# Kernel optimization log

Measured on AMD Instinct MI355X. Metric: run time of the kernel, lower is better.

The kernel has to match this reference:

```python
import jax, jax.numpy as jnp
import numpy as np

N = 200000          # number of nodes (objects)
H = 64              # hidden_size
ARITIES = [1, 2, 3] # arity per relation
NTUP = [250000, 250000, 250000]  # ground atoms per relation


def setup_inputs() -> dict:
    key = jax.random.key(0)
    ks = jax.random.split(key, 32)
    inp = {"node_states": jax.random.normal(ks[0], (N, H), jnp.float32)}
    i = 1
    for r, (a, t) in enumerate(zip(ARITIES, NTUP)):
        inp[f"rel{r}_idx"] = jax.random.randint(ks[i], (t * a,), 0, N, dtype=jnp.int32).astype(jnp.int64); i += 1
        d = a * H
        s = (2.0 / d) ** 0.5
        inp[f"w1_r{r}"] = jax.random.normal(ks[i], (d, d), jnp.float32) * s; i += 1
        inp[f"b1_r{r}"] = jnp.zeros((d,), jnp.float32)
        inp[f"w2_r{r}"] = jax.random.normal(ks[i], (d, d), jnp.float32) * s; i += 1
        inp[f"b2_r{r}"] = jnp.zeros((d,), jnp.float32)
    su = (1.0 / (2 * H)) ** 0.5
    inp["wu1"] = jax.random.normal(ks[i], (2 * H, 2 * H), jnp.float32) * su; i += 1
    inp["bu1"] = jnp.zeros((2 * H,), jnp.float32)
    inp["wu2"] = jax.random.normal(ks[i], (2 * H, H), jnp.float32) * su
    inp["bu2"] = jnp.zeros((H,), jnp.float32)
    return inp


def reference(node_states, rel0_idx, rel1_idx, rel2_idx,
              w1_r0, b1_r0, w2_r0, b2_r0,
              w1_r1, b1_r1, w2_r1, b2_r1,
              w1_r2, b1_r2, w2_r2, b2_r2,
              wu1, bu1, wu2, bu2):
    sum_msg = jnp.zeros_like(node_states)
    rels = [(ARITIES[0], rel0_idx, w1_r0, b1_r0, w2_r0, b2_r0),
            (ARITIES[1], rel1_idx, w1_r1, b1_r1, w2_r1, b2_r1),
            (ARITIES[2], rel2_idx, w1_r2, b1_r2, w2_r2, b2_r2)]
    for a, idx, w1, b1, w2, b2 in rels:
        # gather node states for each ground atom: [T, a*H]
        x = node_states[idx].reshape(-1, a * H)
        h = jax.nn.relu(x @ w1 + b1)
        msg = (h @ w2 + b2).reshape(-1, H)  # [T*a, H]
        # scatter-add messages back to their nodes
        sum_msg = sum_msg.at[idx].add(msg)
    z = jnp.concatenate([sum_msg, node_states], axis=1)  # [N, 2H]
    return jax.nn.relu(z @ wu1 + bu1) @ wu2 + bu2
```

## Files before the change

kernel.cpp:

```cpp
#include <hip/hip_runtime.h>

#define H 64

typedef __attribute__((ext_vector_type(8))) __bf16 bf16x8;
typedef __attribute__((ext_vector_type(4))) float f32x4;
typedef unsigned short u16;
typedef unsigned int u32;

union F8 { bf16x8 b; u16 u[8]; uint4 q; };

__device__ __forceinline__ u16 f2bf(float f) {
    union { __bf16 h; u16 u; } v; v.h = (__bf16)f; return v.u;
}
__device__ __forceinline__ float bf2f(u16 x) {
    return __uint_as_float((u32)x << 16);
}
__device__ __forceinline__ unsigned swz(int col, int k, int K) {
    return ((unsigned)(col * K + k) * 2u) ^ (((unsigned)col & 7u) << 4);
}

struct Seg { const float* src; unsigned dstBytes; int K; int N; };
struct Segs { Seg s[8]; };

__global__ __launch_bounds__(256) void conv_weights(Segs segs, char* out) {
    Seg sg = segs.s[blockIdx.y];
    int total = sg.K * sg.N;
    char* dst = out + sg.dstBytes;
    for (int e = blockIdx.x * 256 + threadIdx.x; e < total; e += gridDim.x * 256) {
        int k = e / sg.N, n = e % sg.N;
        *(u16*)(dst + swz(n, k, sg.K)) = f2bf(sg.src[e]);
    }
}

__global__ __launch_bounds__(256) void conv_nodes(const float4* __restrict__ src,
                                                  ushort4* __restrict__ dst, int n4) {
    for (int i = blockIdx.x * 256 + threadIdx.x; i < n4; i += gridDim.x * 256) {
        float4 f = src[i];
        ushort4 o;
        o.x = f2bf(f.x); o.y = f2bf(f.y); o.z = f2bf(f.z); o.w = f2bf(f.w);
        dst[i] = o;
    }
}

__global__ __launch_bounds__(512) void scan_blocks(u32* __restrict__ data,
                                                   u32* __restrict__ sums, int n) {
    __shared__ u32 s[512];
    int tid = threadIdx.x, i = blockIdx.x * 512 + tid;
    u32 v = (i < n) ? data[i] : 0u;
    s[tid] = v; __syncthreads();
    for (int d = 1; d < 512; d <<= 1) {
        u32 t = (tid >= d) ? s[tid - d] : 0u; __syncthreads();
        s[tid] += t; __syncthreads();
    }
    if (i < n) data[i] = s[tid] - v;
    if (tid == 511) sums[blockIdx.x] = s[511];
}

__global__ __launch_bounds__(512) void scan_sums(u32* __restrict__ sums, int nb) {
    __shared__ u32 s[512];
    int tid = threadIdx.x;
    u32 v = (tid < nb) ? sums[tid] : 0u;
    s[tid] = v; __syncthreads();
    for (int d = 1; d < 512; d <<= 1) {
        u32 t = (tid >= d) ? s[tid - d] : 0u; __syncthreads();
        s[tid] += t; __syncthreads();
    }
    if (tid < nb) sums[tid] = s[tid] - v;
}

__global__ __launch_bounds__(512) void scan_add(u32* __restrict__ data,
                                                const u32* __restrict__ sums, int n) {
    int i = blockIdx.x * 512 + threadIdx.x;
    if (i < n) data[i] += sums[blockIdx.x];
}

struct OFix {
    const int* idx0; const int* idx1; const int* idx2;
    int m0, m1, m2;
    const u32* base; const u32* pre; u32* ord;
};

__global__ __launch_bounds__(256) void ord_fix(OFix a) {
    const int Mtot = a.m0 + a.m1 + a.m2;
    for (int e = blockIdx.x * 256 + threadIdx.x; e < Mtot; e += gridDim.x * 256) {
        int lm = e, node;
        if (lm < a.m0) node = a.idx0[lm];
        else { lm -= a.m0; if (lm < a.m1) node = a.idx1[lm]; else node = a.idx2[lm - a.m1]; }
        a.ord[a.base[node] + a.pre[e]] = (u32)e;
    }
}

struct Scat {
    const int* idx0; const int* idx1; const int* idx2;
    int m0, m1, m2;
    const u32* base; const u32* pre;
    const u16* msgu; u16* msgs;
};

__global__ __launch_bounds__(256) void scatter_msg(Scat a) {
    const int Mtot = a.m0 + a.m1 + a.m2;
    const int CH = Mtot * 8;
    for (int c = blockIdx.x * 256 + threadIdx.x; c < CH; c += gridDim.x * 256) {
        const int e = c >> 3, q = c & 7;
        int lm = e, node;
        if (lm < a.m0) node = a.idx0[lm];
        else { lm -= a.m0; if (lm < a.m1) node = a.idx1[lm]; else node = a.idx2[lm - a.m1]; }
        const u32 slot = a.base[node] + a.pre[e];
        ((uint4*)(a.msgs + (size_t)slot * 64))[q] =
            ((const uint4*)(a.msgu + (size_t)e * 64))[q];
    }
}

template<int A>
__device__ __forceinline__ void msg_body(
    const u16* __restrict__ nsb, const int* __restrict__ idx,
    const u16* __restrict__ w1T, const float* __restrict__ b1,
    const u16* __restrict__ w2T, const float* __restrict__ b2,
    u16* __restrict__ msgR, int T, int bid, u16* Wl, u16* h1)
{
    constexpr int D    = A * 64;
    constexpr int KS   = D / 32;
    constexpr int NT   = D / 16;
    constexpr bool DUAL = (A == 1);
    constexpr bool CS   = (A > 1);
    constexpr int RF   = CS ? 2 : 1;
    constexpr int WH   = (A == 3) ? 3 : 1;
    constexpr int NTH  = NT / WH;
    constexpr int NTW  = CS ? NTH / 2 : NTH;
    constexpr int COLH = D / WH;
    constexpr int NPF  = (DUAL ? 2 * D * D : COLH * D) / 8 / 512;
    constexpr int NB   = WH * NTW;

    const int tid  = threadIdx.x;
    const int lane = tid & 63;
    const int w    = tid >> 6;
    const int g    = lane >> 4;
    const int lr   = lane & 15;
    const int rg   = CS ? (w >> 1) : w;
    const int cg   = CS ? (w & 1) : 0;

    const int tile = bid * 128;

    auto stage = [&](const u16* gsrc) {
#pragma unroll
        for (int i = 0; i < NPF; ++i) {
            const u16* gp = gsrc + ((i * 512 + tid) << 3);
            u16* lp = Wl + ((i * 512 + (w << 6)) << 3);
            __builtin_amdgcn_global_load_lds(
                (const __attribute__((address_space(1))) void*)gp,
                (__attribute__((address_space(3))) void*)lp, 16, 0, 0);
        }
    };

    bf16x8 a1[RF][KS];
#pragma unroll
    for (int rf = 0; rf < RF; ++rf) {
        const int trow = tile + rg * (16 * RF) + rf * 16 + lr;
        const int tl   = trow < T ? trow : T - 1;
        int nodes[A];
#pragma unroll
        for (int s = 0; s < A; ++s) nodes[s] = idx[(long)tl * A + s];
#pragma unroll
        for (int kk = 0; kk < KS; ++kk) {
            const u16* p = nsb + (long)nodes[kk >> 1] * H + ((kk & 1) * 32 + g * 8);
            F8 t; t.q = *(const uint4*)p;
            a1[rf][kk] = t.b;
        }
    }

    float bias1[NB], bias2[NB];
#pragma unroll
    for (int i = 0; i < NB; ++i) {
        const int jg = (i / NTW) * NTH + cg * NTW + (i % NTW);
        bias1[i] = b1[jg * 16 + lr];
        bias2[i] = b2[jg * 16 + lr];
    }

#pragma unroll
    for (int hh = 0; hh < WH; ++hh) {
        stage(DUAL ? w1T : (w1T + (size_t)hh * COLH * D));
        asm volatile("s_waitcnt vmcnt(0)" ::: "memory");
        __syncthreads();

#pragma unroll
        for (int jl = 0; jl < NTW; ++jl) {
            const int jc = cg * NTW + jl;
            const int jg = hh * NTH + jc;
            f32x4 acc0 = {0.f, 0.f, 0.f, 0.f};
            f32x4 acc1 = {0.f, 0.f, 0.f, 0.f};
#pragma unroll
            for (int kk = 0; kk < KS; ++kk) {
                F8 bf; bf.q = *(const uint4*)((const char*)Wl + swz(jc * 16 + lr, kk * 32 + g * 8, D));
                acc0 = __builtin_amdgcn_mfma_f32_16x16x32_bf16(a1[0][kk], bf.b, acc0, 0, 0, 0);
                if constexpr (CS)
                    acc1 = __builtin_amdgcn_mfma_f32_16x16x32_bf16(a1[1][kk], bf.b, acc1, 0, 0, 0);
            }
#pragma unroll
            for (int r = 0; r < 4; ++r) {
                const int row0 = rg * (16 * RF) + g * 4 + r;
                float v0 = acc0[r] + bias1[hh * NTW + jl]; v0 = v0 > 0.f ? v0 : 0.f;
                *(u16*)((char*)h1 + swz(row0, jg * 16 + lr, D)) = f2bf(v0);
                if constexpr (CS) {
                    float v1 = acc1[r] + bias1[hh * NTW + jl]; v1 = v1 > 0.f ? v1 : 0.f;
                    *(u16*)((char*)h1 + swz(row0 + 16, jg * 16 + lr, D)) = f2bf(v1);
                }
            }
        }
        if constexpr (!DUAL) __syncthreads();
    }

    bf16x8 a2[RF][KS];
#pragma unroll
    for (int rf = 0; rf < RF; ++rf) {
        const int row = rg * (16 * RF) + rf * 16 + lr;
#pragma unroll
        for (int kk = 0; kk < KS; ++kk) {
            F8 t; t.q = *(const uint4*)((const char*)h1 + swz(row, kk * 32 + g * 8, D));
            a2[rf][kk] = t.b;
        }
    }

#pragma unroll
    for (int hh = 0; hh < WH; ++hh) {
        if constexpr (!DUAL) {
            stage(w2T + (size_t)hh * COLH * D);
            asm volatile("s_waitcnt vmcnt(0)" ::: "memory");
            __syncthreads();
        }
        const char* W2base = DUAL ? (const char*)(Wl + D * D) : (const char*)Wl;

#pragma unroll
        for (int jl = 0; jl < NTW; ++jl) {
            const int jc = cg * NTW + jl;
            const int jg = hh * NTH + jc;
            f32x4 acc0 = {0.f, 0.f, 0.f, 0.f};
            f32x4 acc1 = {0.f, 0.f, 0.f, 0.f};
#pragma unroll
            for (int kk = 0; kk < KS; ++kk) {
                F8 bf; bf.q = *(const uint4*)(W2base + swz(jc * 16 + lr, kk * 32 + g * 8, D));
                acc0 = __builtin_amdgcn_mfma_f32_16x16x32_bf16(a2[0][kk], bf.b, acc0, 0, 0, 0);
                if constexpr (CS)
                    acc1 = __builtin_amdgcn_mfma_f32_16x16x32_bf16(a2[1][kk], bf.b, acc1, 0, 0, 0);
            }
            const int gc   = jg * 16 + lr;
            const int slot = gc >> 6;
            const int cs_  = gc & 63;
#pragma unroll
            for (int r = 0; r < 4; ++r) {
                const int a0 = rg * (16 * RF) + g * 4 + r;
                const int m0 = a0 * A + slot;
                unsigned b0 = (((unsigned)(m0 * 64 + cs_)) * 2u) ^ (((unsigned)m0 & 7u) << 4);
                *(u16*)((char*)h1 + b0) = f2bf(acc0[r] + bias2[hh * NTW + jl]);
                if constexpr (CS) {
                    const int m1 = (a0 + 16) * A + slot;
                    unsigned b1x = (((unsigned)(m1 * 64 + cs_)) * 2u) ^ (((unsigned)m1 & 7u) << 4);
                    *(u16*)((char*)h1 + b1x) = f2bf(acc1[r] + bias2[hh * NTW + jl]);
                }
            }
        }
        if constexpr (!DUAL) { if (hh + 1 < WH) __syncthreads(); }
    }

    if constexpr (CS) {
        __syncthreads();
        const int mbase = tile * A;
        constexpr int CH = 128 * A * 16;
#pragma unroll
        for (int i = 0; i < CH / 512; ++i) {
            const int c    = i * 512 + tid;
            const int row  = c >> 4;
            const int atom = row / A;
            if (tile + atom < T) {
                unsigned byte = (((unsigned)(row * 64 + (c & 15) * 4)) * 2u) ^ (((unsigned)row & 7u) << 4);
                uint2 v = *(const uint2*)((const char*)h1 + byte);
                *(uint2*)(msgR + (size_t)(mbase + row) * 64 + (c & 15) * 4) = v;
            }
        }
    } else {
        const bool full  = (tile + 128 <= T);
#pragma unroll
        for (int i = 0; i < 16 * A; i += 4) {
            int ml   = i + (lane >> 4);
            int mrow = w * 16 * A + ml;
            bool ok  = full || ((tile + w * 16 + ml / A) < T);
            if (ok) {
                unsigned byte = (((unsigned)(mrow * 64 + (lane & 15) * 4)) * 2u) ^ (((unsigned)mrow & 7u) << 4);
                uint2 v = *(const uint2*)((const char*)h1 + byte);
                *(uint2*)(msgR + (size_t)((tile * A) + mrow) * 64 + (lane & 15) * 4) = v;
            }
        }
    }
}

struct MegaA {
    const u16* nsb;
    const int* idx0; const int* idx1; const int* idx2;
    int m0, m1, m2, t0, t1, t2;
    u32* cnt; u32* pre;
    const u16 *w10, *w20, *w11, *w21, *w12, *w22;
    const float *b10, *b20, *b11, *b21, *b12, *b22;
    u16* msgu;
    int nrank, nb2, nb1, nb0, striped;
};

__global__ __launch_bounds__(512, 4) void mega_kernel(MegaA a) {
    __shared__ __align__(16) u16 sm[36864];
    const int bx = blockIdx.x;
    int kind, id;
    if (a.striped) {
        const int strip = 4 * a.nrank;
        if (bx < strip) {
            if ((bx & 3) == 3) { kind = 1; id = bx >> 2; }
            else               { kind = 0; id = bx - (bx >> 2); }
        } else { kind = 0; id = bx - a.nrank; }
    } else {
        if (bx < a.nrank) { kind = 1; id = bx; }
        else              { kind = 0; id = bx - a.nrank; }
    }

    if (kind == 1) {
        const int Mtot = a.m0 + a.m1 + a.m2;
        for (int e = id * 512 + (int)threadIdx.x; e < Mtot; e += a.nrank * 512) {
            int lm = e, node;
            if (lm < a.m0) node = a.idx0[lm];
            else { lm -= a.m0; if (lm < a.m1) node = a.idx1[lm]; else node = a.idx2[lm - a.m1]; }
            a.pre[e] = atomicAdd(a.cnt + node, 1u);
        }
        return;
    }

    const int nmsg = a.nb2 + a.nb1 + a.nb0;
    if (id >= nmsg) return;
    if (id < a.nb2)
        msg_body<3>(a.nsb, a.idx2, a.w12, a.b12, a.w22, a.b22,
                    a.msgu + (size_t)(a.m0 + a.m1) * 64, a.t2, id, sm, sm + 12288);
    else if (id < a.nb2 + a.nb1)
        msg_body<2>(a.nsb, a.idx1, a.w11, a.b11, a.w21, a.b21,
                    a.msgu + (size_t)a.m0 * 64, a.t1, id - a.nb2, sm, sm + 16384);
    else
        msg_body<1>(a.nsb, a.idx0, a.w10, a.b10, a.w20, a.b20,
                    a.msgu, a.t0, id - a.nb2 - a.nb1, sm, sm + 8192);
}

template<int A>
__global__ __launch_bounds__(512) void rel_kernel(
    const float* __restrict__ ns, const int* __restrict__ idx,
    const u16* __restrict__ w1T, const float* __restrict__ b1,
    const u16* __restrict__ w2T, const float* __restrict__ b2,
    float* __restrict__ dout, int T)
{
    constexpr int D  = A * 64;
    constexpr int KS = D / 32;
    constexpr int NT = D / 16;
    constexpr bool DUAL = (A == 1);
    __shared__ __align__(16) u16 Wl[(DUAL ? 2 : 1) * D * D];
    __shared__ __align__(16) u16 h1[128 * D];

    const int tid  = threadIdx.x;
    const int lane = tid & 63;
    const int w    = tid >> 6;
    const int g    = lane >> 4;
    const int lr   = lane & 15;

    const int tile = blockIdx.x * 128;
    const int trow = tile + w * 16 + lr;
    const int tl   = trow < T ? trow : T - 1;

    {
        constexpr int NV = (DUAL ? 2 : 1) * D * D / 8;
        const uint4* s4 = (const uint4*)w1T;
        uint4* d4 = (uint4*)Wl;
#pragma unroll
        for (int i = 0; i < NV / 512; ++i) d4[i * 512 + tid] = s4[i * 512 + tid];
    }

    int nodes[A];
#pragma unroll
    for (int s = 0; s < A; ++s) nodes[s] = idx[(long)tl * A + s];

    bf16x8 a1[KS];
#pragma unroll
    for (int kk = 0; kk < KS; ++kk) {
        const float* p = ns + (long)nodes[kk >> 1] * H + ((kk & 1) * 32 + g * 8);
        float4 f0 = *(const float4*)p;
        float4 f1 = *(const float4*)(p + 4);
        F8 t;
        t.u[0] = f2bf(f0.x); t.u[1] = f2bf(f0.y); t.u[2] = f2bf(f0.z); t.u[3] = f2bf(f0.w);
        t.u[4] = f2bf(f1.x); t.u[5] = f2bf(f1.y); t.u[6] = f2bf(f1.z); t.u[7] = f2bf(f1.w);
        a1[kk] = t.b;
    }

    float bias1[NT];
#pragma unroll
    for (int j = 0; j < NT; ++j) bias1[j] = b1[j * 16 + lr];

    __syncthreads();

#pragma unroll
    for (int j = 0; j < NT; ++j) {
        f32x4 acc = {0.f, 0.f, 0.f, 0.f};
#pragma unroll
        for (int kk = 0; kk < KS; ++kk) {
            F8 bf; bf.q = *(const uint4*)((const char*)Wl + swz(j * 16 + lr, kk * 32 + g * 8, D));
            acc = __builtin_amdgcn_mfma_f32_16x16x32_bf16(a1[kk], bf.b, acc, 0, 0, 0);
        }
#pragma unroll
        for (int r = 0; r < 4; ++r) {
            float vv = acc[r] + bias1[j];
            vv = vv > 0.f ? vv : 0.f;
            int row = w * 16 + g * 4 + r;
            *(u16*)((char*)h1 + swz(row, j * 16 + lr, D)) = f2bf(vv);
        }
    }

    const char* W2base;
    if constexpr (!DUAL) {
        __syncthreads();
        const uint4* s4 = (const uint4*)w2T;
        uint4* d4 = (uint4*)Wl;
        constexpr int NV = D * D / 8;
#pragma unroll
        for (int i = 0; i < NV / 512; ++i) d4[i * 512 + tid] = s4[i * 512 + tid];
        W2base = (const char*)Wl;
    } else {
        W2base = (const char*)(Wl + D * D);
    }

    bf16x8 a2[KS];
#pragma unroll
    for (int kk = 0; kk < KS; ++kk) {
        int row = w * 16 + lr;
        F8 t; t.q = *(const uint4*)((const char*)h1 + swz(row, kk * 32 + g * 8, D));
        a2[kk] = t.b;
    }

    float bias2[NT];
#pragma unroll
    for (int j = 0; j < NT; ++j) bias2[j] = b2[j * 16 + lr];

    int  nodes2[A][4];
    bool pred[4];
#pragma unroll
    for (int r = 0; r < 4; ++r) {
        int t  = tile + w * 16 + g * 4 + r;
        int tc = t < T ? t : T - 1;
        pred[r] = t < T;
#pragma unroll
        for (int s = 0; s < A; ++s) nodes2[s][r] = idx[(long)tc * A + s];
    }
    if constexpr (!DUAL) __syncthreads();

#pragma unroll
    for (int j = 0; j < NT; ++j) {
        f32x4 acc = {0.f, 0.f, 0.f, 0.f};
#pragma unroll
        for (int kk = 0; kk < KS; ++kk) {
            F8 bf; bf.q = *(const uint4*)(W2base + swz(j * 16 + lr, kk * 32 + g * 8, D));
            acc = __builtin_amdgcn_mfma_f32_16x16x32_bf16(a2[kk], bf.b, acc, 0, 0, 0);
        }
        const int slot = j >> 2;
        const int coff = (j & 3) * 16 + lr;
#pragma unroll
        for (int r = 0; r < 4; ++r) {
            if (pred[r])
                unsafeAtomicAdd(dout + (long)nodes2[slot][r] * H + coff, acc[r] + bias2[j]);
        }
    }
}

template<int MODE>
__global__ __launch_bounds__(512) void update_kernel(
    const float* __restrict__ ns, const u16* __restrict__ nsb,
    const float* __restrict__ sum,
    const u32* __restrict__ ord, const u32* __restrict__ base,
    const u16* __restrict__ msg, int Mtot,
    const u16* __restrict__ wu1T, const float* __restrict__ bu1,
    const u16* __restrict__ wu2T, const float* __restrict__ bu2,
    float* __restrict__ out, int N)
{
    __shared__ __align__(16) u16 Wl[128 * 128 + 64 * 128];
    __shared__ __align__(16) u16 h[128 * 128];

    const int tid  = threadIdx.x;
    const int lane = tid & 63;
    const int w    = tid >> 6;
    const int g    = lane >> 4;
    const int lr   = lane & 15;

    {
        const uint4* s4 = (const uint4*)wu1T;
        uint4* d4 = (uint4*)Wl;
#pragma unroll
        for (int i = 0; i < 6; ++i) d4[i * 512 + tid] = s4[i * 512 + tid];
    }

    const int tile = blockIdx.x * 128;
    const int trow = tile + w * 16 + lr;
    const int tl   = trow < N ? trow : N - 1;

    bf16x8 a1[4];
    if constexpr (MODE <= 1) {
        const u32 s = base[tl];
        const u32 e = (tl + 1 < N) ? base[tl + 1] : (u32)Mtot;
        float s0[8], s1[8];
#pragma unroll
        for (int j = 0; j < 8; ++j) { s0[j] = 0.f; s1[j] = 0.f; }
        for (u32 p = s; p < e; ++p) {
            const u16* row = msg + (size_t)(MODE == 1 ? ord[p] : p) * 64;
            F8 v0, v1;
            v0.q = *(const uint4*)(row + g * 8);
            v1.q = *(const uint4*)(row + 32 + g * 8);
#pragma unroll
            for (int j = 0; j < 8; ++j) { s0[j] += bf2f(v0.u[j]); s1[j] += bf2f(v1.u[j]); }
        }
        F8 t0, t1;
#pragma unroll
        for (int j = 0; j < 8; ++j) { t0.u[j] = f2bf(s0[j]); t1.u[j] = f2bf(s1[j]); }
        a1[0] = t0.b; a1[1] = t1.b;
    } else {
#pragma unroll
        for (int kk = 0; kk < 2; ++kk) {
            int k = kk * 32 + g * 8;
            const float* p = sum + (long)tl * H + k;
            float4 f0 = *(const float4*)p;
            float4 f1 = *(const float4*)(p + 4);
            F8 t;
            t.u[0] = f2bf(f0.x); t.u[1] = f2bf(f0.y); t.u[2] = f2bf(f0.z); t.u[3] = f2bf(f0.w);
            t.u[4] = f2bf(f1.x); t.u[5] = f2bf(f1.y); t.u[6] = f2bf(f1.z); t.u[7] = f2bf(f1.w);
            a1[kk] = t.b;
        }
    }
#pragma unroll
    for (int kk = 2; kk < 4; ++kk) {
        if constexpr (MODE <= 1) {
            const u16* prow = nsb + (long)tl * H;
            F8 t; t.q = *(const uint4*)(prow + (kk - 2) * 32 + g * 8);
            a1[kk] = t.b;
        } else {
            int k = (kk - 2) * 32 + g * 8;
            const float* p = ns + (long)tl * H + k;
            float4 f0 = *(const float4*)p;
            float4 f1 = *(const float4*)(p + 4);
            F8 t;
            t.u[0] = f2bf(f0.x); t.u[1] = f2bf(f0.y); t.u[2] = f2bf(f0.z); t.u[3] = f2bf(f0.w);
            t.u[4] = f2bf(f1.x); t.u[5] = f2bf(f1.y); t.u[6] = f2bf(f1.z); t.u[7] = f2bf(f1.w);
            a1[kk] = t.b;
        }
    }

    float bias1[8], bias2[4];
#pragma unroll
    for (int j = 0; j < 8; ++j) bias1[j] = bu1[j * 16 + lr];
#pragma unroll
    for (int j = 0; j < 4; ++j) bias2[j] = bu2[j * 16 + lr];

    __syncthreads();

#pragma unroll
    for (int j = 0; j < 8; ++j) {
        f32x4 acc = {0.f, 0.f, 0.f, 0.f};
#pragma unroll
        for (int kk = 0; kk < 4; ++kk) {
            F8 bf; bf.q = *(const uint4*)((const char*)Wl + swz(j * 16 + lr, kk * 32 + g * 8, 128));
            acc = __builtin_amdgcn_mfma_f32_16x16x32_bf16(a1[kk], bf.b, acc, 0, 0, 0);
        }
#pragma unroll
        for (int r = 0; r < 4; ++r) {
            float vv = acc[r] + bias1[j];
            vv = vv > 0.f ? vv : 0.f;
            int row = w * 16 + g * 4 + r;
            *(u16*)((char*)h + swz(row, j * 16 + lr, 128)) = f2bf(vv);
        }
    }

    bf16x8 a2[4];
#pragma unroll
    for (int kk = 0; kk < 4; ++kk) {
        int row = w * 16 + lr;
        F8 t; t.q = *(const uint4*)((const char*)h + swz(row, kk * 32 + g * 8, 128));
        a2[kk] = t.b;
    }

    const char* W2base = (const char*)(Wl + 128 * 128);
#pragma unroll
    for (int j = 0; j < 4; ++j) {
        f32x4 acc = {0.f, 0.f, 0.f, 0.f};
#pragma unroll
        for (int kk = 0; kk < 4; ++kk) {
            F8 bf; bf.q = *(const uint4*)(W2base + swz(j * 16 + lr, kk * 32 + g * 8, 128));
            acc = __builtin_amdgcn_mfma_f32_16x16x32_bf16(a2[kk], bf.b, acc, 0, 0, 0);
        }
#pragma unroll
        for (int r = 0; r < 4; ++r) {
            int t = tile + w * 16 + g * 4 + r;
            if (t < N) out[(long)t * H + j * 16 + lr] = acc[r] + bias2[j];
        }
    }
}

extern "C" void kernel_launch(void* const* d_in, const int* in_sizes, int n_in,
                              void* d_out, int out_size, void* d_ws, size_t ws_size,
                              hipStream_t stream) {
    const float* ns = (const float*)d_in[0];
    const int* idxs[3] = { (const int*)d_in[1], (const int*)d_in[6], (const int*)d_in[11] };
    const float* b1s[3] = { (const float*)d_in[3], (const float*)d_in[8], (const float*)d_in[13] };
    const float* b2s[3] = { (const float*)d_in[5], (const float*)d_in[10], (const float*)d_in[15] };
    const float* bu1 = (const float*)d_in[17];
    const float* bu2 = (const float*)d_in[19];

    const int N = in_sizes[0] / H;
    const int Ts[3] = { in_sizes[1], in_sizes[6] / 2, in_sizes[11] / 3 };
    const int Ms[3] = { Ts[0] * 1, Ts[1] * 2, Ts[2] * 3 };
    const long Mtot = (long)Ms[0] + Ms[1] + Ms[2];

    char* wsb = (char*)d_ws;
    auto AL = [](size_t x) { return (x + 255) & ~(size_t)255; };

    const unsigned O_W1R0 = 0;
    const unsigned O_W2R0 = O_W1R0 + 64 * 64 * 2;
    const unsigned O_W1R1 = O_W2R0 + 64 * 64 * 2;
    const unsigned O_W2R1 = O_W1R1 + 128 * 128 * 2;
    const unsigned O_W1R2 = O_W2R1 + 128 * 128 * 2;
    const unsigned O_W2R2 = O_W1R2 + 192 * 192 * 2;
    const unsigned O_WU1  = O_W2R2 + 192 * 192 * 2;
    const unsigned O_WU2  = O_WU1 + 128 * 128 * 2;
    const size_t  wEnd    = O_WU2 + 128 * 64 * 2;
    const unsigned wOff1[3] = { O_W1R0, O_W1R1, O_W1R2 };
    const unsigned wOff2[3] = { O_W2R0, O_W2R1, O_W2R2 };

    const int nb = (N + 511) / 512;

    const size_t O_CNT = AL(wEnd);
    const size_t O_SUM = AL(O_CNT + (size_t)N * 4);
    const size_t O_PRE = AL(O_SUM + (size_t)nb * 4);
    const size_t O_ORD = AL(O_PRE + (size_t)Mtot * 4);
    const size_t O_NSB = AL(O_ORD + (size_t)Mtot * 4);
    const size_t nsLen = (size_t)N * H * 2;
    const size_t O_MSG = AL(O_NSB + nsLen);
    const size_t O_MSGS = AL(O_MSG + (size_t)Mtot * 128);
    const size_t need1 = O_MSGS;
    const size_t need2 = O_MSGS + (size_t)Mtot * 128;

    const bool sorted2 = (nb <= 512) && (ws_size >= need2);
    const bool sorted1 = (nb <= 512) && (ws_size >= need1);

    Segs segs;
    segs.s[0] = {(const float*)d_in[2],  O_W1R0, 64, 64};
    segs.s[1] = {(const float*)d_in[4],  O_W2R0, 64, 64};
    segs.s[2] = {(const float*)d_in[7],  O_W1R1, 128, 128};
    segs.s[3] = {(const float*)d_in[9],  O_W2R1, 128, 128};
    segs.s[4] = {(const float*)d_in[12], O_W1R2, 192, 192};
    segs.s[5] = {(const float*)d_in[14], O_W2R2, 192, 192};
    segs.s[6] = {(const float*)d_in[16], O_WU1, 128, 128};
    segs.s[7] = {(const float*)d_in[18], O_WU2, 128, 64};

    float* dout = (float*)d_out;
    const u16* W1[3] = { (const u16*)(wsb + wOff1[0]), (const u16*)(wsb + wOff1[1]), (const u16*)(wsb + wOff1[2]) };
    const u16* W2[3] = { (const u16*)(wsb + wOff2[0]), (const u16*)(wsb + wOff2[1]), (const u16*)(wsb + wOff2[2]) };

    auto gT = [](int T) { return (T + 127) / 128; };

    if (sorted1 || sorted2) {
        u32* cnt = (u32*)(wsb + O_CNT);
        u32* sums = (u32*)(wsb + O_SUM);
        u32* pre = (u32*)(wsb + O_PRE);
        u32* ord = (u32*)(wsb + O_ORD);
        u16* nsbp = (u16*)(wsb + O_NSB);
        u16* msgu = (u16*)(wsb + O_MSG);
        u16* msgs = (u16*)(wsb + O_MSGS);

        hipMemsetAsync(cnt, 0, (size_t)N * 4, stream);
        conv_weights<<<dim3(36, 8), 256, 0, stream>>>(segs, wsb);
        conv_nodes<<<1024, 256, 0, stream>>>((const float4*)ns, (ushort4*)nsbp, N * H / 4);

        const int nb0 = gT(Ts[0]), nb1 = gT(Ts[1]), nb2 = gT(Ts[2]);
        const int nmsg = nb0 + nb1 + nb2;
        int NR = nmsg / 3; if (NR > 1024) NR = 1024; if (NR < 1) NR = 1;
        const int striped = (nmsg >= 3 * NR) ? 1 : 0;
        const int NTOT = NR + nmsg;

        MegaA ma;
        ma.nsb = nsbp;
        ma.idx0 = idxs[0]; ma.idx1 = idxs[1]; ma.idx2 = idxs[2];
        ma.m0 = Ms[0]; ma.m1 = Ms[1]; ma.m2 = Ms[2];
        ma.t0 = Ts[0]; ma.t1 = Ts[1]; ma.t2 = Ts[2];
        ma.cnt = cnt; ma.pre = pre;
        ma.w10 = W1[0]; ma.w20 = W2[0];
        ma.w11 = W1[1]; ma.w21 = W2[1];
        ma.w12 = W1[2]; ma.w22 = W2[2];
        ma.b10 = b1s[0]; ma.b20 = b2s[0];
        ma.b11 = b1s[1]; ma.b21 = b2s[1];
        ma.b12 = b1s[2]; ma.b22 = b2s[2];
        ma.msgu = msgu;
        ma.nrank = NR; ma.nb2 = nb2; ma.nb1 = nb1; ma.nb0 = nb0; ma.striped = striped;
        mega_kernel<<<NTOT, 512, 0, stream>>>(ma);

        scan_blocks<<<nb, 512, 0, stream>>>(cnt, sums, N);
        scan_sums<<<1, 512, 0, stream>>>(sums, nb);
        scan_add<<<nb, 512, 0, stream>>>(cnt, sums, N);

        if (sorted2) {
            Scat sc;
            sc.idx0 = idxs[0]; sc.idx1 = idxs[1]; sc.idx2 = idxs[2];
            sc.m0 = Ms[0]; sc.m1 = Ms[1]; sc.m2 = Ms[2];
            sc.base = cnt; sc.pre = pre;
            sc.msgu = msgu; sc.msgs = msgs;
            scatter_msg<<<2048, 256, 0, stream>>>(sc);

            update_kernel<0><<<(N + 127) / 128, 512, 0, stream>>>(
                ns, nsbp, nullptr, nullptr, cnt, msgs, (int)Mtot,
                (const u16*)(wsb + O_WU1), bu1, (const u16*)(wsb + O_WU2), bu2, dout, N);
        } else {
            OFix fx;
            fx.idx0 = idxs[0]; fx.idx1 = idxs[1]; fx.idx2 = idxs[2];
            fx.m0 = Ms[0]; fx.m1 = Ms[1]; fx.m2 = Ms[2];
            fx.base = cnt; fx.pre = pre; fx.ord = ord;
            ord_fix<<<2048, 256, 0, stream>>>(fx);

            update_kernel<1><<<(N + 127) / 128, 512, 0, stream>>>(
                ns, nsbp, nullptr, ord, cnt, msgu, (int)Mtot,
                (const u16*)(wsb + O_WU1), bu1, (const u16*)(wsb + O_WU2), bu2, dout, N);
        }
    } else {
        conv_weights<<<dim3(36, 8), 256, 0, stream>>>(segs, wsb);
        hipMemsetAsync(dout, 0, (size_t)N * H * sizeof(float), stream);
        for (int r = 0; r < 3; ++r) {
            const int T = Ts[r], nbl = gT(T);
            if (r == 0) rel_kernel<1><<<nbl, 512, 0, stream>>>(ns, idxs[0], W1[0], b1s[0], W2[0], b2s[0], dout, T);
            if (r == 1) rel_kernel<2><<<nbl, 512, 0, stream>>>(ns, idxs[1], W1[1], b1s[1], W2[1], b2s[1], dout, T);
            if (r == 2) rel_kernel<3><<<nbl, 512, 0, stream>>>(ns, idxs[2], W1[2], b1s[2], W2[2], b2s[2], dout, T);
        }
        update_kernel<2><<<(N + 127) / 128, 512, 0, stream>>>(
            ns, nullptr, dout, nullptr, nullptr, nullptr, 0,
            (const u16*)(wsb + O_WU1), bu1, (const u16*)(wsb + O_WU2), bu2, dout, N);
    }
}
```

Baseline: 269.9 us.

## Restructure arity-2/3 message MLP into K-chunked tiles and fuse prep kernels

Merges the memset, weight conversion and node conversion into one prep kernel to cut launch overhead. Changes the weight layout to 64-wide K-chunks (swzK) and restructures the arity-2/3 message MLP so each warp group computes a 64-row by quarter-column tile, streaming weights in 64-row K-chunks through smaller LDS. The arity-1 path is specialised separately. This lowers LDS footprint and raises B-fragment reuse across four row fragments, at the cost of more register pressure and extra barriers per chunk.

New measurement: 332.6 us. 1.23x slower.

```diff
diff --git a/kernel.cpp b/kernel.cpp
--- a/kernel.cpp
+++ b/kernel.cpp
@@ -17,6 +17,10 @@
 }
 __device__ __forceinline__ unsigned swz(int col, int k, int K) {
     return ((unsigned)(col * K + k) * 2u) ^ (((unsigned)col & 7u) << 4);
+}
+__device__ __forceinline__ unsigned swzK(int col, int k, int N) {
+    return (unsigned)(k >> 6) * ((unsigned)N * 128u)
+         + ((((unsigned)(col * 64 + (k & 63))) * 2u) ^ (((unsigned)col & 7u) << 4));
 }
 
 struct Seg { const float* src; unsigned dstBytes; int K; int N; };
@@ -28,17 +32,33 @@
     char* dst = out + sg.dstBytes;
     for (int e = blockIdx.x * 256 + threadIdx.x; e < total; e += gridDim.x * 256) {
         int k = e / sg.N, n = e % sg.N;
-        *(u16*)(dst + swz(n, k, sg.K)) = f2bf(sg.src[e]);
-    }
-}
-
-__global__ __launch_bounds__(256) void conv_nodes(const float4* __restrict__ src,
-                                                  ushort4* __restrict__ dst, int n4) {
-    for (int i = blockIdx.x * 256 + threadIdx.x; i < n4; i += gridDim.x * 256) {
-        float4 f = src[i];
-        ushort4 o;
-        o.x = f2bf(f.x); o.y = f2bf(f.y); o.z = f2bf(f.z); o.w = f2bf(f.w);
-        dst[i] = o;
+        *(u16*)(dst + swzK(n, k, sg.N)) = f2bf(sg.src[e]);
+    }
+}
+
+struct PrepA { const float4* nsrc; ushort4* ndst; int n4; Segs segs; char* wout; u32* cnt; int N; };
+
+__global__ __launch_bounds__(256) void prep_kernel(PrepA a) {
+    if (blockIdx.y == 0) {
+        for (int i = blockIdx.x * 256 + threadIdx.x; i < a.n4; i += gridDim.x * 256) {
+            float4 f = a.nsrc[i];
+            ushort4 o;
+            o.x = f2bf(f.x); o.y = f2bf(f.y); o.z = f2bf(f.z); o.w = f2bf(f.w);
+            a.ndst[i] = o;
+        }
+    } else if (blockIdx.y == 1) {
+        for (int s = 0; s < 8; ++s) {
+            Seg sg = a.segs.s[s];
+            int total = sg.K * sg.N;
+            char* dst = a.wout + sg.dstBytes;
+            for (int e = blockIdx.x * 256 + threadIdx.x; e < total; e += gridDim.x * 256) {
+                int k = e / sg.N, n = e % sg.N;
+                *(u16*)(dst + swzK(n, k, sg.N)) = f2bf(sg.src[e]);
+            }
+        }
+    } else {
+        for (int i = blockIdx.x * 256 + threadIdx.x; i < a.N; i += gridDim.x * 256)
+            a.cnt[i] = 0u;
     }
 }
 
@@ -118,151 +138,231 @@
     const u16* __restrict__ w2T, const float* __restrict__ b2,
     u16* __restrict__ msgR, int T, int bid, u16* Wl, u16* h1)
 {
-    constexpr int D    = A * 64;
-    constexpr int KS   = D / 32;
-    constexpr int NT   = D / 16;
-    constexpr bool DUAL = (A == 1);
-    constexpr bool CS   = (A > 1);
-    constexpr int RF   = CS ? 2 : 1;
-    constexpr int WH   = (A == 3) ? 3 : 1;
-    constexpr int NTH  = NT / WH;
-    constexpr int NTW  = CS ? NTH / 2 : NTH;
-    constexpr int COLH = D / WH;
-    constexpr int NPF  = (DUAL ? 2 * D * D : COLH * D) / 8 / 512;
-    constexpr int NB   = WH * NTW;
+    constexpr int D  = A * 64;
+    constexpr int NT = D / 16;
 
     const int tid  = threadIdx.x;
     const int lane = tid & 63;
     const int w    = tid >> 6;
     const int g    = lane >> 4;
     const int lr   = lane & 15;
-    const int rg   = CS ? (w >> 1) : w;
-    const int cg   = CS ? (w & 1) : 0;
-
     const int tile = bid * 128;
 
-    auto stage = [&](const u16* gsrc) {
-#pragma unroll
-        for (int i = 0; i < NPF; ++i) {
-            const u16* gp = gsrc + ((i * 512 + tid) << 3);
-            u16* lp = Wl + ((i * 512 + (w << 6)) << 3);
-            __builtin_amdgcn_global_load_lds(
-                (const __attribute__((address_space(1))) void*)gp,
-                (__attribute__((address_space(3))) void*)lp, 16, 0, 0);
-        }
-    };
-
-    bf16x8 a1[RF][KS];
-#pragma unroll
-    for (int rf = 0; rf < RF; ++rf) {
-        const int trow = tile + rg * (16 * RF) + rf * 16 + lr;
+    if constexpr (A == 1) {
+        constexpr int KS = 2;
+        constexpr int NPF = 2 * D * D / 8 / 512;
+        const int trow = tile + w * 16 + lr;
         const int tl   = trow < T ? trow : T - 1;
-        int nodes[A];
-#pragma unroll
-        for (int s = 0; s < A; ++s) nodes[s] = idx[(long)tl * A + s];
+
+        {
+#pragma unroll
+            for (int i = 0; i < NPF; ++i) {
+                const u16* gp = w1T + ((i * 512 + tid) << 3);
+                u16* lp = Wl + ((i * 512 + (w << 6)) << 3);
+                __builtin_amdgcn_global_load_lds(
+                    (const __attribute__((address_space(1))) void*)gp,
+                    (__attribute__((address_space(3))) void*)lp, 16, 0, 0);
+            }
+        }
+
+        const int node = idx[tl];
+        bf16x8 a1[KS];
 #pragma unroll
         for (int kk = 0; kk < KS; ++kk) {
-            const u16* p = nsb + (long)nodes[kk >> 1] * H + ((kk & 1) * 32 + g * 8);
+            const u16* p = nsb + (long)node * H + kk * 32 + g * 8;
             F8 t; t.q = *(const uint4*)p;
-            a1[rf][kk] = t.b;
-        }
-    }
-
-    float bias1[NB], bias2[NB];
-#pragma unroll
-    for (int i = 0; i < NB; ++i) {
-        const int jg = (i / NTW) * NTH + cg * NTW + (i % NTW);
-        bias1[i] = b1[jg * 16 + lr];
-        bias2[i] = b2[jg * 16 + lr];
-    }
-
-#pragma unroll
-    for (int hh = 0; hh < WH; ++hh) {
-        stage(DUAL ? w1T : (w1T + (size_t)hh * COLH * D));
+            a1[kk] = t.b;
+        }
+
+        float bias1[NT], bias2[NT];
+#pragma unroll
+        for (int j = 0; j < NT; ++j) bias1[j] = b1[j * 16 + lr];
+#pragma unroll
+        for (int j = 0; j < NT; ++j) bias2[j] = b2[j * 16 + lr];
+
         asm volatile("s_waitcnt vmcnt(0)" ::: "memory");
         __syncthreads();
 
 #pragma unroll
+        for (int j = 0; j < NT; ++j) {
+            f32x4 acc = {0.f, 0.f, 0.f, 0.f};
+#pragma unroll
+            for (int kk = 0; kk < KS; ++kk) {
+                F8 bf; bf.q = *(const uint4*)((const char*)Wl + swz(j * 16 + lr, kk * 32 + g * 8, D));
+                acc = __builtin_amdgcn_mfma_f32_16x16x32_bf16(a1[kk], bf.b, acc, 0, 0, 0);
+            }
+#pragma unroll
+            for (int r = 0; r < 4; ++r) {
+                float vv = acc[r] + bias1[j];
+                vv = vv > 0.f ? vv : 0.f;
+                int row = w * 16 + g * 4 + r;
+                *(u16*)((char*)h1 + swz(row, j * 16 + lr, D)) = f2bf(vv);
+            }
+        }
+
+        bf16x8 a2[KS];
+#pragma unroll
+        for (int kk = 0; kk < KS; ++kk) {
+            int row = w * 16 + lr;
+            F8 t; t.q = *(const uint4*)((const char*)h1 + swz(row, kk * 32 + g * 8, D));
+            a2[kk] = t.b;
+        }
+        const char* W2base = (const char*)(Wl + D * D);
+
+#pragma unroll
+        for (int j = 0; j < NT; ++j) {
+            f32x4 acc = {0.f, 0.f, 0.f, 0.f};
+#pragma unroll
+            for (int kk = 0; kk < KS; ++kk) {
+                F8 bf; bf.q = *(const uint4*)(W2base + swz(j * 16 + lr, kk * 32 + g * 8, D));
+                acc = __builtin_amdgcn_mfma_f32_16x16x32_bf16(a2[kk], bf.b, acc, 0, 0, 0);
+            }
+            const int cs_ = j * 16 + lr;
+#pragma unroll
+            for (int r = 0; r < 4; ++r) {
+                int mrow = w * 16 + g * 4 + r;
+                unsigned byte = (((unsigned)(mrow * 64 + cs_)) * 2u) ^ (((unsigned)mrow & 7u) << 4);
+                *(u16*)((char*)h1 + byte) = f2bf(acc[r] + bias2[j]);
+            }
+        }
+
+        const bool full = (tile + 128 <= T);
+#pragma unroll
+        for (int i = 0; i < 16; i += 4) {
+            int ml   = i + (lane >> 4);
+            int mrow = w * 16 + ml;
+            bool ok  = full || ((tile + mrow) < T);
+            if (ok) {
+                unsigned byte = (((unsigned)(mrow * 64 + (lane & 15) * 4)) * 2u) ^ (((unsigned)mrow & 7u) << 4);
+                uint2 v = *(const uint2*)((const char*)h1 + byte);
+                *(uint2*)(msgR + (size_t)(tile + mrow) * 64 + (lane & 15) * 4) = v;
+            }
+        }
+    } else {
+        constexpr int NC  = A;
+        constexpr int CG  = 4;
+        constexpr int RF  = 4;
+        constexpr int NTW = NT / CG;
+        constexpr int NPF = D * 64 * 2 / 16 / 512;
+
+        const int rg = w >> 2;
+        const int cg = w & 3;
+        const int c0 = cg * (NTW * 16);
+
+        auto stage = [&](const u16* gsrc) {
+#pragma unroll
+            for (int i = 0; i < NPF; ++i) {
+                const u16* gp = gsrc + ((i * 512 + tid) << 3);
+                u16* lp = Wl + ((i * 512 + (w << 6)) << 3);
+                __builtin_amdgcn_global_load_lds(
+                    (const __attribute__((address_space(1))) void*)gp,
+                    (__attribute__((address_space(3))) void*)lp, 16, 0, 0);
+            }
+        };
+
+        int tl[RF];
+#pragma unroll
+        for (int rf = 0; rf < RF; ++rf) {
+            int trow = tile + rg * 64 + rf * 16 + lr;
+            tl[rf] = trow < T ? trow : T - 1;
+        }
+
+        float bias1[NTW], bias2[NTW];
+#pragma unroll
         for (int jl = 0; jl < NTW; ++jl) {
-            const int jc = cg * NTW + jl;
-            const int jg = hh * NTH + jc;
-            f32x4 acc0 = {0.f, 0.f, 0.f, 0.f};
-            f32x4 acc1 = {0.f, 0.f, 0.f, 0.f};
-#pragma unroll
-            for (int kk = 0; kk < KS; ++kk) {
-                F8 bf; bf.q = *(const uint4*)((const char*)Wl + swz(jc * 16 + lr, kk * 32 + g * 8, D));
-                acc0 = __builtin_amdgcn_mfma_f32_16x16x32_bf16(a1[0][kk], bf.b, acc0, 0, 0, 0);
-                if constexpr (CS)
-                    acc1 = __builtin_amdgcn_mfma_f32_16x16x32_bf16(a1[1][kk], bf.b, acc1, 0, 0, 0);
-            }
-#pragma unroll
-            for (int r = 0; r < 4; ++r) {
-                const int row0 = rg * (16 * RF) + g * 4 + r;
-                float v0 = acc0[r] + bias1[hh * NTW + jl]; v0 = v0 > 0.f ? v0 : 0.f;
-                *(u16*)((char*)h1 + swz(row0, jg * 16 + lr, D)) = f2bf(v0);
-                if constexpr (CS) {
-                    float v1 = acc1[r] + bias1[hh * NTW + jl]; v1 = v1 > 0.f ? v1 : 0.f;
-                    *(u16*)((char*)h1 + swz(row0 + 16, jg * 16 + lr, D)) = f2bf(v1);
-                }
-            }
-        }
-        if constexpr (!DUAL) __syncthreads();
-    }
-
-    bf16x8 a2[RF][KS];
-#pragma unroll
-    for (int rf = 0; rf < RF; ++rf) {
-        const int row = rg * (16 * RF) + rf * 16 + lr;
-#pragma unroll
-        for (int kk = 0; kk < KS; ++kk) {
-            F8 t; t.q = *(const uint4*)((const char*)h1 + swz(row, kk * 32 + g * 8, D));
-            a2[rf][kk] = t.b;
-        }
-    }
-
-#pragma unroll
-    for (int hh = 0; hh < WH; ++hh) {
-        if constexpr (!DUAL) {
-            stage(w2T + (size_t)hh * COLH * D);
+            bias1[jl] = b1[c0 + jl * 16 + lr];
+            bias2[jl] = b2[c0 + jl * 16 + lr];
+        }
+
+        f32x4 acc[NTW][RF];
+#pragma unroll
+        for (int jl = 0; jl < NTW; ++jl)
+#pragma unroll
+            for (int rf = 0; rf < RF; ++rf) acc[jl][rf] = f32x4{0.f, 0.f, 0.f, 0.f};
+
+#pragma unroll
+        for (int kc = 0; kc < NC; ++kc) {
+            stage(w1T + (size_t)kc * D * 64);
+            bf16x8 a1[RF][2];
+#pragma unroll
+            for (int rf = 0; rf < RF; ++rf) {
+                const int node = idx[(long)tl[rf] * A + kc];
+                const u16* p = nsb + (long)node * H + g * 8;
+                F8 t0; t0.q = *(const uint4*)p;        a1[rf][0] = t0.b;
+                F8 t1; t1.q = *(const uint4*)(p + 32); a1[rf][1] = t1.b;
+            }
             asm volatile("s_waitcnt vmcnt(0)" ::: "memory");
             __syncthreads();
-        }
-        const char* W2base = DUAL ? (const char*)(Wl + D * D) : (const char*)Wl;
+#pragma unroll
+            for (int jl = 0; jl < NTW; ++jl)
+#pragma unroll
+                for (int kl = 0; kl < 2; ++kl) {
+                    F8 bf; bf.q = *(const uint4*)((const char*)Wl + swz(c0 + jl * 16 + lr, kl * 32 + g * 8, 64));
+#pragma unroll
+                    for (int rf = 0; rf < RF; ++rf)
+                        acc[jl][rf] = __builtin_amdgcn_mfma_f32_16x16x32_bf16(a1[rf][kl], bf.b, acc[jl][rf], 0, 0, 0);
+                }
+            __syncthreads();
+        }
+
+#pragma unroll
+        for (int jl = 0; jl < NTW; ++jl)
+#pragma unroll
+            for (int rf = 0; rf < RF; ++rf)
+#pragma unroll
+                for (int r = 0; r < 4; ++r) {
+                    float v = acc[jl][rf][r] + bias1[jl];
+                    v = v > 0.f ? v : 0.f;
+                    const int row = rg * 64 + rf * 16 + g * 4 + r;
+                    *(u16*)((char*)h1 + swz(row, c0 + jl * 16 + lr, D)) = f2bf(v);
+                    acc[jl][rf][r] = 0.f;
+                }
+        __syncthreads();
+
+#pragma unroll
+        for (int kc = 0; kc < NC; ++kc) {
+            stage(w2T + (size_t)kc * D * 64);
+            bf16x8 a2[RF][2];
+#pragma unroll
+            for (int rf = 0; rf < RF; ++rf) {
+                const int row = rg * 64 + rf * 16 + lr;
+#pragma unroll
+                for (int kl = 0; kl < 2; ++kl) {
+                    F8 t; t.q = *(const uint4*)((const char*)h1 + swz(row, kc * 64 + kl * 32 + g * 8, D));
+                    a2[rf][kl] = t.b;
+                }
+            }
+            asm volatile("s_waitcnt vmcnt(0)" ::: "memory");
+            __syncthreads();
+#pragma unroll
+            for (int jl = 0; jl < NTW; ++jl)
+#pragma unroll
+                for (int kl = 0; kl < 2; ++kl) {
+                    F8 bf; bf.q = *(const uint4*)((const char*)Wl + swz(c0 + jl * 16 + lr, kl * 32 + g * 8, 64));
+#pragma unroll
+                    for (int rf = 0; rf < RF; ++rf)
+                        acc[jl][rf] = __builtin_amdgcn_mfma_f32_16x16x32_bf16(a2[rf][kl], bf.b, acc[jl][rf], 0, 0, 0);
+                }
+            if (kc + 1 < NC) __syncthreads();
+        }
 
 #pragma unroll
         for (int jl = 0; jl < NTW; ++jl) {
-            const int jc = cg * NTW + jl;
-            const int jg = hh * NTH + jc;
-            f32x4 acc0 = {0.f, 0.f, 0.f, 0.f};
-            f32x4 acc1 = {0.f, 0.f, 0.f, 0.f};
-#pragma unroll
-            for (int kk = 0; kk < KS; ++kk) {
-                F8 bf; bf.q = *(const uint4*)(W2base + swz(jc * 16 + lr, kk * 32 + g * 8, D));
-                acc0 = __builtin_amdgcn_mfma_f32_16x16x32_bf16(a2[0][kk], bf.b, acc0, 0, 0, 0);
-                if constexpr (CS)
-                    acc1 = __builtin_amdgcn_mfma_f32_16x16x32_bf16(a2[1][kk], bf.b, acc1, 0, 0, 0);
-            }
-            const int gc   = jg * 16 + lr;
+            const int gc   = c0 + jl * 16 + lr;
             const int slot = gc >> 6;
             const int cs_  = gc & 63;
 #pragma unroll
-            for (int r = 0; r < 4; ++r) {
-                const int a0 = rg * (16 * RF) + g * 4 + r;
-                const int m0 = a0 * A + slot;
-                unsigned b0 = (((unsigned)(m0 * 64 + cs_)) * 2u) ^ (((unsigned)m0 & 7u) << 4);
-                *(u16*)((char*)h1 + b0) = f2bf(acc0[r] + bias2[hh * NTW + jl]);
-                if constexpr (CS) {
-                    const int m1 = (a0 + 16) * A + slot;
-                    unsigned b1x = (((unsigned)(m1 * 64 + cs_)) * 2u) ^ (((unsigned)m1 & 7u) << 4);
-                    *(u16*)((char*)h1 + b1x) = f2bf(acc1[r] + bias2[hh * NTW + jl]);
+            for (int rf = 0; rf < RF; ++rf)
+#pragma unroll
+                for (int r = 0; r < 4; ++r) {
+                    const int a0 = rg * 64 + rf * 16 + g * 4 + r;
+                    const int m0 = a0 * A + slot;
+                    unsigned b0 = (((unsigned)(m0 * 64 + cs_)) * 2u) ^ (((unsigned)m0 & 7u) << 4);
+                    *(u16*)((char*)h1 + b0) = f2bf(acc[jl][rf][r] + bias2[jl]);
                 }
-            }
-        }
-        if constexpr (!DUAL) { if (hh + 1 < WH) __syncthreads(); }
-    }
-
-    if constexpr (CS) {
+        }
         __syncthreads();
+
         const int mbase = tile * A;
         constexpr int CH = 128 * A * 16;
 #pragma unroll
@@ -274,19 +374,6 @@
                 unsigned byte = (((unsigned)(row * 64 + (c & 15) * 4)) * 2u) ^ (((unsigned)row & 7u) << 4);
                 uint2 v = *(const uint2*)((const char*)h1 + byte);
                 *(uint2*)(msgR + (size_t)(mbase + row) * 64 + (c & 15) * 4) = v;
-            }
-        }
-    } else {
-        const bool full  = (tile + 128 <= T);
-#pragma unroll
-        for (int i = 0; i < 16 * A; i += 4) {
-            int ml   = i + (lane >> 4);
-            int mrow = w * 16 * A + ml;
-            bool ok  = full || ((tile + w * 16 + ml / A) < T);
-            if (ok) {
-                unsigned byte = (((unsigned)(mrow * 64 + (lane & 15) * 4)) * 2u) ^ (((unsigned)mrow & 7u) << 4);
-                uint2 v = *(const uint2*)((const char*)h1 + byte);
-                *(uint2*)(msgR + (size_t)((tile * A) + mrow) * 64 + (lane & 15) * 4) = v;
             }
         }
     }
@@ -336,7 +423,7 @@
                     a.msgu + (size_t)(a.m0 + a.m1) * 64, a.t2, id, sm, sm + 12288);
     else if (id < a.nb2 + a.nb1)
         msg_body<2>(a.nsb, a.idx1, a.w11, a.b11, a.w21, a.b21,
-                    a.msgu + (size_t)a.m0 * 64, a.t1, id - a.nb2, sm, sm + 16384);
+                    a.msgu + (size_t)a.m0 * 64, a.t1, id - a.nb2, sm, sm + 8192);
     else
         msg_body<1>(a.nsb, a.idx0, a.w10, a.b10, a.w20, a.b20,
                     a.msgu, a.t0, id - a.nb2 - a.nb1, sm, sm + 8192);
@@ -401,7 +488,7 @@
         f32x4 acc = {0.f, 0.f, 0.f, 0.f};
 #pragma unroll
         for (int kk = 0; kk < KS; ++kk) {
-            F8 bf; bf.q = *(const uint4*)((const char*)Wl + swz(j * 16 + lr, kk * 32 + g * 8, D));
+            F8 bf; bf.q = *(const uint4*)((const char*)Wl + swzK(j * 16 + lr, kk * 32 + g * 8, D));
             acc = __builtin_amdgcn_mfma_f32_16x16x32_bf16(a1[kk], bf.b, acc, 0, 0, 0);
         }
 #pragma unroll
@@ -455,7 +542,7 @@
         f32x4 acc = {0.f, 0.f, 0.f, 0.f};
 #pragma unroll
         for (int kk = 0; kk < KS; ++kk) {
-            F8 bf; bf.q = *(const uint4*)(W2base + swz(j * 16 + lr, kk * 32 + g * 8, D));
+            F8 bf; bf.q = *(const uint4*)(W2base + swzK(j * 16 + lr, kk * 32 + g * 8, D));
             acc = __builtin_amdgcn_mfma_f32_16x16x32_bf16(a2[kk], bf.b, acc, 0, 0, 0);
         }
         const int slot = j >> 2;
@@ -561,7 +648,7 @@
         f32x4 acc = {0.f, 0.f, 0.f, 0.f};
 #pragma unroll
         for (int kk = 0; kk < 4; ++kk) {
-            F8 bf; bf.q = *(const uint4*)((const char*)Wl + swz(j * 16 + lr, kk * 32 + g * 8, 128));
+            F8 bf; bf.q = *(const uint4*)((const char*)Wl + swzK(j * 16 + lr, kk * 32 + g * 8, 128));
             acc = __builtin_amdgcn_mfma_f32_16x16x32_bf16(a1[kk], bf.b, acc, 0, 0, 0);
         }
 #pragma unroll
@@ -587,7 +674,7 @@
         f32x4 acc = {0.f, 0.f, 0.f, 0.f};
 #pragma unroll
         for (int kk = 0; kk < 4; ++kk) {
-            F8 bf; bf.q = *(const uint4*)(W2base + swz(j * 16 + lr, kk * 32 + g * 8, 128));
+            F8 bf; bf.q = *(const uint4*)(W2base + swzK(j * 16 + lr, kk * 32 + g * 8, 64));
             acc = __builtin_amdgcn_mfma_f32_16x16x32_bf16(a2[kk], bf.b, acc, 0, 0, 0);
         }
 #pragma unroll
@@ -669,9 +756,10 @@
         u16* msgu = (u16*)(wsb + O_MSG);
         u16* msgs = (u16*)(wsb + O_MSGS);
 
-        hipMemsetAsync(cnt, 0, (size_t)N * 4, stream);
-        conv_weights<<<dim3(36, 8), 256, 0, stream>>>(segs, wsb);
-        conv_nodes<<<1024, 256, 0, stream>>>((const float4*)ns, (ushort4*)nsbp, N * H / 4);
+        PrepA pp;
+        pp.nsrc = (const float4*)ns; pp.ndst = (ushort4*)nsbp; pp.n4 = N * H / 4;
+        pp.segs = segs; pp.wout = wsb; pp.cnt = cnt; pp.N = N;
+        prep_kernel<<<dim3(448, 3), 256, 0, stream>>>(pp);
 
         const int nb0 = gT(Ts[0]), nb1 = gT(Ts[1]), nb2 = gT(Ts[2]);
         const int nmsg = nb0 + nb1 + nb2;
```
